# Optimization experiments

Measured on AMD Instinct MI355X. Metric: run time of the kernel, lower is better.

Reference implementation:

```python
import jax, jax.numpy as jnp
import numpy as np

B = 4096        # batch_size
D = 256         # feature_dim
N = 9000000     # dataset size (state buffer length)
G = 100         # num_groups
ALPHA = 0.5     # alpha_weight
GAMMA = 0.8
RHO = 8.0
LAM = 1.0       # lambada
ETA_P = 0.01
EPS = 1e-14
CLIP = 5.0


def setup_inputs() -> dict:
    key = jax.random.key(0)
    k = jax.random.split(key, 6)
    zis = jax.random.normal(k[0], (B, D), jnp.float32)
    zjs = jax.random.normal(k[1], (B, D), jnp.float32)
    # per-sample learned temperatures, small positive values
    taus_I = 0.01 + 0.2 * jax.random.uniform(k[2], (N,), jnp.float32)
    taus_T = 0.01 + 0.2 * jax.random.uniform(k[3], (N,), jnp.float32)
    group_info_I = jax.random.randint(k[4], (N,), 0, G, dtype=jnp.int32)
    group_info_T = jax.random.randint(k[5], (N,), 0, G, dtype=jnp.int32)
    ids = jnp.arange(B, dtype=jnp.int32)  # unique sample indices
    zeros_N = jnp.zeros((N,), jnp.float32)
    return {
        "zis": zis, "zjs": zjs,
        "s_I": zeros_N, "s_T": zeros_N, "b_I": zeros_N, "b_T": zeros_N,
        "z_I": jnp.zeros((G,), jnp.float32), "z_T": jnp.zeros((G,), jnp.float32),
        "p_I": jnp.ones((G,), jnp.float32) / G, "p_T": jnp.ones((G,), jnp.float32) / G,
        "taus_I": taus_I, "taus_T": taus_T,
        "ids": ids, "group_info_I": group_info_I, "group_info_T": group_info_T,
    }


def _l2norm(x):
    return x / jnp.maximum(jnp.linalg.norm(x, axis=1, keepdims=True), 1e-12)


def reference(zis, zjs, s_I, s_T, b_I, b_T, z_I, z_T, p_I, p_T,
              taus_I, taus_T, ids, group_info_I, group_info_T):
    zis = _l2norm(zis)
    zjs = _l2norm(zjs)
    sim = zis @ zjs.T                                   # [B, B]
    diag = jnp.diagonal(sim)                            # [B]
    mask_neg = 1.0 - jnp.eye(B, dtype=sim.dtype)
    image_diffs = sim - diag[:, None]
    text_diffs = sim - diag[None, :]

    tau_I = taus_I[ids]                                 # [B]
    tau_T = taus_T[ids]
    idt = jax.lax.stop_gradient(image_diffs / tau_I[:, None])
    tdt = jax.lax.stop_gradient(text_diffs / tau_T[None, :])

    # running max state (numerically-stable exp)
    old_b_I = b_I[ids]
    b_I_new = jnp.maximum(jnp.max(idt, axis=1), old_b_I)    # [B]
    old_b_T = b_T[ids]
    b_T_new = jnp.maximum(jnp.max(tdt, axis=0), old_b_T)    # [B]
    b_I = b_I.at[ids].set(b_I_new)
    b_T = b_T.at[ids].set(b_T_new)

    exp_I = jnp.exp(idt - b_I_new[:, None]) * mask_neg
    exp_T = jnp.exp(tdt - b_T_new[None, :]) * mask_neg
    g_I = jnp.sum(exp_I, axis=1)                         # [B]
    g_T = jnp.sum(exp_T, axis=0)                         # [B]

    # EMA of softmax denominators with max-rescaling
    s_I_new = (1.0 - GAMMA) * s_I[ids] * jnp.exp(old_b_I - b_I_new) + GAMMA * g_I
    s_T_new = (1.0 - GAMMA) * s_T[ids] * jnp.exp(old_b_T - b_T_new) + GAMMA * g_T
    s_I = s_I.at[ids].set(s_I_new)
    s_T = s_T.at[ids].set(s_T_new)
    s_I_c = jnp.maximum(s_I_new, EPS)
    s_T_c = jnp.maximum(s_T_new, EPS)

    w_I = exp_I / s_I_c[:, None]
    w_T = exp_T / s_T_c[None, :]

    gid_I = group_info_I[ids]                            # [B]
    gid_T = group_info_T[ids]
    gw_I = G * p_I[gid_I]                                # [B]
    gw_T = G * p_T[gid_T]

    image_loss = jnp.sum(w_I * gw_I[:, None] * image_diffs, axis=1)   # [B]
    text_loss = jnp.sum(w_T * gw_T[None, :] * text_diffs, axis=0)     # [B]
    total_loss = ALPHA * image_loss.mean() + (1.0 - ALPHA) * text_loss.mean()

    # per-group adversarial weight update
    F_I = tau_I * (jnp.log(s_I_c) + b_I_new + RHO)       # [B]
    F_T = tau_T * (jnp.log(s_T_c) + b_T_new + RHO)
    ones_b = jnp.ones((B,), sim.dtype)
    cnt_I = jnp.maximum(jax.ops.segment_sum(ones_b, gid_I, num_segments=G), 1.0)
    cnt_T = jnp.maximum(jax.ops.segment_sum(ones_b, gid_T, num_segments=G), 1.0)
    grad_p_I = jax.ops.segment_sum(F_I, gid_I, num_segments=G) / cnt_I
    grad_p_T = jax.ops.segment_sum(F_T, gid_T, num_segments=G) / cnt_T

    z_I = (1.0 - GAMMA) * z_I + GAMMA * grad_p_I
    z_T = (1.0 - GAMMA) * z_T + GAMMA * grad_p_T
    grad_hp_I = -LAM * jnp.log(p_I + EPS) - LAM
    grad_hp_T = -LAM * jnp.log(p_T + EPS) - LAM
    new_p_I = p_I * jnp.exp(2.0 * ETA_P * jnp.clip(z_I + grad_hp_I, -CLIP, CLIP))
    new_p_T = p_T * jnp.exp(2.0 * ETA_P * jnp.clip(z_T + grad_hp_T, -CLIP, CLIP))
    p_I = new_p_I / new_p_I.sum()
    p_T = new_p_T / new_p_T.sum()

    return total_loss, p_I, p_T
```

## Files before the change

kernel.cpp:

```cpp
#include <hip/hip_runtime.h>
#include <hip/hip_bf16.h>
#include <math.h>

#define BB 4096
#define DD 256
#define GG 100
#define GAMMA_C 0.8f
#define RHO_C 8.0f
#define ALPHA_C 0.5f
#define EPS_C 1e-14f
#define NS2 64

typedef __bf16 bf16x8 __attribute__((ext_vector_type(8)));
typedef float f32x4 __attribute__((ext_vector_type(4)));

__device__ inline void gl2lds16(const void* g, void* l) {
    __builtin_amdgcn_global_load_lds((__attribute__((address_space(1))) void*)(void*)g,
                                     (__attribute__((address_space(3))) void*)l, 16, 0, 0);
}

__device__ inline float blockReduceSum(float v, float* lds) {
    for (int o = 32; o > 0; o >>= 1) v += __shfl_down(v, o);
    int lane = threadIdx.x & 63, wid = threadIdx.x >> 6;
    if (lane == 0) lds[wid] = v;
    __syncthreads();
    if (threadIdx.x == 0) {
        float r = lds[0];
        int nw = blockDim.x >> 6;
        for (int w = 1; w < nw; w++) r += lds[w];
        lds[0] = r;
    }
    __syncthreads();
    float r = lds[0];
    __syncthreads();
    return r;
}

__global__ void norm_kernel(const float* __restrict__ zis,
                            const float* __restrict__ zjs,
                            ushort* __restrict__ zhi, ushort* __restrict__ zlo,
                            ushort* __restrict__ whi, ushort* __restrict__ wlo,
                            float* __restrict__ diag, float* __restrict__ acc) {
    __shared__ float lds[8];
    int r = blockIdx.x;
    if (r == 0) { acc[threadIdx.x] = 0.f; acc[threadIdx.x + 256] = 0.f; }
    float zv = zis[r * DD + threadIdx.x];
    float wv = zjs[r * DD + threadIdx.x];
    float sz = blockReduceSum(zv * zv, lds);
    float sw = blockReduceSum(wv * wv, lds);
    float nz = zv * (1.0f / fmaxf(sqrtf(sz), 1e-12f));
    float nw = wv * (1.0f / fmaxf(sqrtf(sw), 1e-12f));
    float dt = blockReduceSum(nz * nw, lds);
    if (threadIdx.x == 0) diag[r] = dt;
    __hip_bfloat16 hz = __float2bfloat16(nz);
    __hip_bfloat16 lz = __float2bfloat16(nz - __bfloat162float(hz));
    __hip_bfloat16 hw = __float2bfloat16(nw);
    __hip_bfloat16 lw = __float2bfloat16(nw - __bfloat162float(hw));
    zhi[r * DD + threadIdx.x] = *(ushort*)&hz;
    zlo[r * DD + threadIdx.x] = *(ushort*)&lz;
    whi[r * DD + threadIdx.x] = *(ushort*)&hw;
    wlo[r * DD + threadIdx.x] = *(ushort*)&lw;
}

__global__ void __launch_bounds__(256) fused_tile(const ushort* __restrict__ Ahi,
        const ushort* __restrict__ Alo, const ushort* __restrict__ Bhi,
        const ushort* __restrict__ Blo, const float* __restrict__ diag,
        const float* __restrict__ tausI, const float* __restrict__ tausT,
        const int* __restrict__ ids,
        float* __restrict__ pmR, float* __restrict__ pgR, float* __restrict__ pwR,
        float* __restrict__ pmC, float* __restrict__ pgC, float* __restrict__ pwC) {
    __shared__ ushort sAhi[128 * 32];
    __shared__ ushort sAlo[128 * 32];
    __shared__ ushort sBhi[128 * 32];
    __shared__ ushort sBlo[128 * 32];
    __shared__ float rDiag[128], rITau[128];
    __shared__ float cDiag[128], cITau[128];

    int lane = threadIdx.x & 63;
    int wv = threadIdx.x >> 6;
    int wm = wv >> 1, wn = wv & 1;
    int bm = blockIdx.y * 128, bn = blockIdx.x * 128;
    int ml = lane & 15, kq = lane >> 4;
    int koff = kq * 8;

    if (threadIdx.x < 128) {
        int r = bm + threadIdx.x;
        rDiag[threadIdx.x] = diag[r];
        rITau[threadIdx.x] = 1.0f / tausI[ids[r]];
    } else {
        int c = bn + threadIdx.x - 128;
        cDiag[threadIdx.x - 128] = diag[c];
        cITau[threadIdx.x - 128] = 1.0f / tausT[ids[c]];
    }

    f32x4 acc[4][4] = {};
    for (int k0 = 0; k0 < DD; k0 += 32) {
        for (int i = 0; i < 2; i++) {
            int cbase = i * 256 + wv * 64;
            int c = cbase + lane;
            int row = c >> 2;
            int col = (c & 3) * 8;
            size_t ga = (size_t)(bm + row) * DD + k0 + col;
            size_t gb = (size_t)(bn + row) * DD + k0 + col;
            int lofs = cbase * 8;
            gl2lds16(&Ahi[ga], &sAhi[lofs]);
            gl2lds16(&Alo[ga], &sAlo[lofs]);
            gl2lds16(&Bhi[gb], &sBhi[lofs]);
            gl2lds16(&Blo[gb], &sBlo[lofs]);
        }
        __syncthreads();
        bf16x8 ah[4], al[4], bh[4], bl[4];
        for (int t = 0; t < 4; t++) {
            int ar = wm * 64 + t * 16 + ml;
            ah[t] = *(const bf16x8*)&sAhi[ar * 32 + koff];
            al[t] = *(const bf16x8*)&sAlo[ar * 32 + koff];
            int br = wn * 64 + t * 16 + ml;
            bh[t] = *(const bf16x8*)&sBhi[br * 32 + koff];
            bl[t] = *(const bf16x8*)&sBlo[br * 32 + koff];
        }
        for (int t = 0; t < 4; t++)
            for (int u = 0; u < 4; u++) {
                acc[t][u] = __builtin_amdgcn_mfma_f32_16x16x32_bf16(ah[t], bh[u], acc[t][u], 0, 0, 0);
                acc[t][u] = __builtin_amdgcn_mfma_f32_16x16x32_bf16(ah[t], bl[u], acc[t][u], 0, 0, 0);
                acc[t][u] = __builtin_amdgcn_mfma_f32_16x16x32_bf16(al[t], bh[u], acc[t][u], 0, 0, 0);
            }
        __syncthreads();
    }

    float rd[4][4], rit[4][4];
    for (int t = 0; t < 4; t++)
        for (int reg = 0; reg < 4; reg++) {
            int rl = wm * 64 + t * 16 + kq * 4 + reg;
            rd[t][reg] = rDiag[rl];
            rit[t][reg] = rITau[rl];
        }
    float blocR[4][4];
    for (int t = 0; t < 4; t++)
        for (int reg = 0; reg < 4; reg++) {
            float m = fmaxf(fmaxf(acc[t][0][reg], acc[t][1][reg]),
                            fmaxf(acc[t][2][reg], acc[t][3][reg]));
            for (int mask = 1; mask <= 8; mask <<= 1)
                m = fmaxf(m, __shfl_xor(m, mask));
            blocR[t][reg] = (m - rd[t][reg]) * rit[t][reg];
        }
    float cd[4], cit[4], cbloc[4];
    for (int u = 0; u < 4; u++) {
        int cl = wn * 64 + u * 16 + ml;
        cd[u] = cDiag[cl];
        cit[u] = cITau[cl];
        float m = -INFINITY;
        for (int t = 0; t < 4; t++)
            for (int reg = 0; reg < 4; reg++)
                m = fmaxf(m, acc[t][u][reg]);
        for (int mask = 16; mask <= 32; mask <<= 1)
            m = fmaxf(m, __shfl_xor(m, mask));
        cbloc[u] = (m - cd[u]) * cit[u];
    }
    float rg[4][4] = {}, rw[4][4] = {}, cg[4] = {}, cw[4] = {};
    for (int t = 0; t < 4; t++) {
        int gr0 = bm + wm * 64 + t * 16 + kq * 4;
        for (int u = 0; u < 4; u++) {
            int gc = bn + wn * 64 + u * 16 + ml;
            for (int reg = 0; reg < 4; reg++) {
                float v = acc[t][u][reg];
                bool off = (gr0 + reg) != gc;
                float dvI = v - rd[t][reg];
                float eI = off ? __expf(dvI * rit[t][reg] - blocR[t][reg]) : 0.f;
                rg[t][reg] += eI;
                rw[t][reg] += eI * dvI;
                float dvT = v - cd[u];
                float eT = off ? __expf(dvT * cit[u] - cbloc[u]) : 0.f;
                cg[u] += eT;
                cw[u] += eT * dvT;
            }
        }
    }
    int stripeR = blockIdx.x * 2 + wn;
    for (int t = 0; t < 4; t++) {
        for (int reg = 0; reg < 4; reg++)
            for (int mask = 1; mask <= 8; mask <<= 1) {
                rg[t][reg] += __shfl_xor(rg[t][reg], mask);
                rw[t][reg] += __shfl_xor(rw[t][reg], mask);
            }
        if (ml == 0) {
            size_t o = (size_t)stripeR * BB + bm + wm * 64 + t * 16 + kq * 4;
            *(float4*)&pmR[o] = make_float4(blocR[t][0], blocR[t][1], blocR[t][2], blocR[t][3]);
            *(float4*)&pgR[o] = make_float4(rg[t][0], rg[t][1], rg[t][2], rg[t][3]);
            *(float4*)&pwR[o] = make_float4(rw[t][0], rw[t][1], rw[t][2], rw[t][3]);
        }
    }
    int stripeC = blockIdx.y * 2 + wm;
    for (int u = 0; u < 4; u++) {
        for (int mask = 16; mask <= 32; mask <<= 1) {
            cg[u] += __shfl_xor(cg[u], mask);
            cw[u] += __shfl_xor(cw[u], mask);
        }
        if (kq == 0) {
            size_t o = (size_t)stripeC * BB + bn + wn * 64 + u * 16 + ml;
            pmC[o] = cbloc[u];
            pgC[o] = cg[u];
            pwC[o] = cw[u];
        }
    }
}

__global__ void __launch_bounds__(256) fin_kernel(
        const float* __restrict__ pmR, const float* __restrict__ pgR,
        const float* __restrict__ pwR, const float* __restrict__ pmC,
        const float* __restrict__ pgC, const float* __restrict__ pwC,
        const float* __restrict__ sI, const float* __restrict__ bI,
        const float* __restrict__ tausI, const int* __restrict__ gInfI,
        const float* __restrict__ pI,
        const float* __restrict__ sT, const float* __restrict__ bT,
        const float* __restrict__ tausT, const int* __restrict__ gInfT,
        const float* __restrict__ pT,
        const int* __restrict__ ids, float* __restrict__ acc) {
    __shared__ float lds[8];
    __shared__ float binF[GG], binC[GG];
    if (threadIdx.x < GG) { binF[threadIdx.x] = 0.f; binC[threadIdx.x] = 0.f; }
    __syncthreads();
    int side = blockIdx.x >> 4;
    int i = (blockIdx.x & 15) * 256 + threadIdx.x;
    const float* pm = side ? pmC : pmR;
    const float* pg = side ? pgC : pgR;
    const float* pw = side ? pwC : pwR;
    const float* sS = side ? sT : sI;
    const float* bS = side ? bT : bI;
    const float* taus = side ? tausT : tausI;
    const int* ginfo = side ? gInfT : gInfI;
    const float* pP = side ? pT : pI;

    int id = ids[i];
    float oldb = bS[id];
    float m = -INFINITY;
    for (int s = 0; s < NS2; s++) m = fmaxf(m, pm[(size_t)s * BB + i]);
    float bfin = fmaxf(m, oldb);
    float g = 0.f, wsum = 0.f;
    for (int s = 0; s < NS2; s++) {
        float f = __expf(pm[(size_t)s * BB + i] - bfin);
        g += pg[(size_t)s * BB + i] * f;
        wsum += pw[(size_t)s * BB + i] * f;
    }
    float tau = taus[id];
    float snew = (1.f - GAMMA_C) * sS[id] * expf(oldb - bfin) + GAMMA_C * g;
    float sc = fmaxf(snew, EPS_C);
    int gid = ginfo[id];
    float gw = (float)GG * pP[gid];
    float loss = gw * wsum / sc;
    float F = tau * (logf(sc) + bfin + RHO_C);
    atomicAdd(&binF[gid], F);
    atomicAdd(&binC[gid], 1.0f);
    float lsum = blockReduceSum(loss, lds);
    if (threadIdx.x == 0) atomicAdd(&acc[side], lsum);
    __syncthreads();
    if (threadIdx.x < GG) {
        atomicAdd(&acc[2 + side * 200 + threadIdx.x], binF[threadIdx.x]);
        atomicAdd(&acc[102 + side * 200 + threadIdx.x], binC[threadIdx.x]);
    }
}

__global__ void final_kernel(const float* __restrict__ acc,
                             const float* __restrict__ zI, const float* __restrict__ zT,
                             const float* __restrict__ pI, const float* __restrict__ pT,
                             float* __restrict__ out) {
    __shared__ float sumsI[2], sumsT[2];
    int g = threadIdx.x;
    float npI = 0.f, npT = 0.f;
    if (g < GG) {
        float cntI = fmaxf(acc[102 + g], 1.f);
        float gpI = acc[2 + g] / cntI;
        float zi = (1.f - GAMMA_C) * zI[g] + GAMMA_C * gpI;
        float ghpI = -logf(pI[g] + EPS_C) - 1.f;
        float ti = fminf(fmaxf(zi + ghpI, -5.f), 5.f);
        npI = pI[g] * expf(0.02f * ti);

        float cntT = fmaxf(acc[302 + g], 1.f);
        float gpT = acc[202 + g] / cntT;
        float zt = (1.f - GAMMA_C) * zT[g] + GAMMA_C * gpT;
        float ghpT = -logf(pT[g] + EPS_C) - 1.f;
        float tt = fminf(fmaxf(zt + ghpT, -5.f), 5.f);
        npT = pT[g] * expf(0.02f * tt);
    }
    float vI = npI, vT = npT;
    for (int o = 32; o > 0; o >>= 1) {
        vI += __shfl_down(vI, o);
        vT += __shfl_down(vT, o);
    }
    int wid = threadIdx.x >> 6, lane = threadIdx.x & 63;
    if (lane == 0) { sumsI[wid] = vI; sumsT[wid] = vT; }
    __syncthreads();
    float sumI = sumsI[0] + sumsI[1];
    float sumT = sumsT[0] + sumsT[1];
    if (g < GG) {
        out[1 + g] = npI / sumI;
        out[101 + g] = npT / sumT;
    }
    if (threadIdx.x == 0) {
        out[0] = ALPHA_C * (acc[0] / (float)BB) + (1.f - ALPHA_C) * (acc[1] / (float)BB);
    }
}

extern "C" void kernel_launch(void* const* d_in, const int* in_sizes, int n_in,
                              void* d_out, int out_size, void* d_ws, size_t ws_size,
                              hipStream_t stream) {
    const float* zis   = (const float*)d_in[0];
    const float* zjs   = (const float*)d_in[1];
    const float* s_I   = (const float*)d_in[2];
    const float* s_T   = (const float*)d_in[3];
    const float* b_I   = (const float*)d_in[4];
    const float* b_T   = (const float*)d_in[5];
    const float* z_I   = (const float*)d_in[6];
    const float* z_T   = (const float*)d_in[7];
    const float* p_I   = (const float*)d_in[8];
    const float* p_T   = (const float*)d_in[9];
    const float* tausI = (const float*)d_in[10];
    const float* tausT = (const float*)d_in[11];
    const int*   ids   = (const int*)d_in[12];
    const int*   gInfI = (const int*)d_in[13];
    const int*   gInfT = (const int*)d_in[14];
    float* out = (float*)d_out;

    char* ws = (char*)d_ws;
    ushort* zhi = (ushort*)ws;
    ushort* zlo = zhi + (size_t)BB * DD;
    ushort* whi = zlo + (size_t)BB * DD;
    ushort* wlo = whi + (size_t)BB * DD;
    float* acc  = (float*)(wlo + (size_t)BB * DD);
    float* diag = acc + 512;
    float* pmR  = diag + BB;
    float* pgR  = pmR + (size_t)NS2 * BB;
    float* pwR  = pgR + (size_t)NS2 * BB;
    float* pmC  = pwR + (size_t)NS2 * BB;
    float* pgC  = pmC + (size_t)NS2 * BB;
    float* pwC  = pgC + (size_t)NS2 * BB;

    norm_kernel<<<BB, 256, 0, stream>>>(zis, zjs, zhi, zlo, whi, wlo, diag, acc);
    fused_tile<<<dim3(32, 32), 256, 0, stream>>>(zhi, zlo, whi, wlo, diag,
            tausI, tausT, ids, pmR, pgR, pwR, pmC, pgC, pwC);
    fin_kernel<<<32, 256, 0, stream>>>(pmR, pgR, pwR, pmC, pgC, pwC,
            s_I, b_I, tausI, gInfI, p_I, s_T, b_T, tausT, gInfT, p_T, ids, acc);
    final_kernel<<<1, 128, 0, stream>>>(acc, z_I, z_T, p_I, p_T, out);
}
```

Baseline: 321.4 us.

## Pre-swizzle bf16 operands into MFMA fragment order and load directly from global

```diff
diff --git a/kernel.cpp b/kernel.cpp
--- a/kernel.cpp
+++ b/kernel.cpp
@@ -14,9 +14,9 @@
 typedef __bf16 bf16x8 __attribute__((ext_vector_type(8)));
 typedef float f32x4 __attribute__((ext_vector_type(4)));
 
-__device__ inline void gl2lds16(const void* g, void* l) {
-    __builtin_amdgcn_global_load_lds((__attribute__((address_space(1))) void*)(void*)g,
-                                     (__attribute__((address_space(3))) void*)l, 16, 0, 0);
+__device__ inline int swz(int r, int k) {
+    return ((r >> 4) << 12) | ((k >> 5) << 9) | (((k >> 3) & 3) << 7) |
+           ((r & 15) << 3) | (k & 7);
 }
 
 __device__ inline float blockReduceSum(float v, float* lds) {
@@ -56,10 +56,11 @@
     __hip_bfloat16 lz = __float2bfloat16(nz - __bfloat162float(hz));
     __hip_bfloat16 hw = __float2bfloat16(nw);
     __hip_bfloat16 lw = __float2bfloat16(nw - __bfloat162float(hw));
-    zhi[r * DD + threadIdx.x] = *(ushort*)&hz;
-    zlo[r * DD + threadIdx.x] = *(ushort*)&lz;
-    whi[r * DD + threadIdx.x] = *(ushort*)&hw;
-    wlo[r * DD + threadIdx.x] = *(ushort*)&lw;
+    int si = swz(r, threadIdx.x);
+    zhi[si] = *(ushort*)&hz;
+    zlo[si] = *(ushort*)&lz;
+    whi[si] = *(ushort*)&hw;
+    wlo[si] = *(ushort*)&lw;
 }
 
 __global__ void __launch_bounds__(256) fused_tile(const ushort* __restrict__ Ahi,
@@ -69,10 +70,6 @@
         const int* __restrict__ ids,
         float* __restrict__ pmR, float* __restrict__ pgR, float* __restrict__ pwR,
         float* __restrict__ pmC, float* __restrict__ pgC, float* __restrict__ pwC) {
-    __shared__ ushort sAhi[128 * 32];
-    __shared__ ushort sAlo[128 * 32];
-    __shared__ ushort sBhi[128 * 32];
-    __shared__ ushort sBlo[128 * 32];
     __shared__ float rDiag[128], rITau[128];
     __shared__ float cDiag[128], cITau[128];
 
@@ -81,7 +78,6 @@
     int wm = wv >> 1, wn = wv & 1;
     int bm = blockIdx.y * 128, bn = blockIdx.x * 128;
     int ml = lane & 15, kq = lane >> 4;
-    int koff = kq * 8;
 
     if (threadIdx.x < 128) {
         int r = bm + threadIdx.x;
@@ -93,39 +89,32 @@
         cITau[threadIdx.x - 128] = 1.0f / tausT[ids[c]];
     }
 
+    int aBlk = (bm >> 4) + wm * 4;
+    int bBlk = (bn >> 4) + wn * 4;
+    int lofs = lane * 8;
+
     f32x4 acc[4][4] = {};
-    for (int k0 = 0; k0 < DD; k0 += 32) {
-        for (int i = 0; i < 2; i++) {
-            int cbase = i * 256 + wv * 64;
-            int c = cbase + lane;
-            int row = c >> 2;
-            int col = (c & 3) * 8;
-            size_t ga = (size_t)(bm + row) * DD + k0 + col;
-            size_t gb = (size_t)(bn + row) * DD + k0 + col;
-            int lofs = cbase * 8;
-            gl2lds16(&Ahi[ga], &sAhi[lofs]);
-            gl2lds16(&Alo[ga], &sAlo[lofs]);
-            gl2lds16(&Bhi[gb], &sBhi[lofs]);
-            gl2lds16(&Blo[gb], &sBlo[lofs]);
-        }
-        __syncthreads();
+#pragma unroll
+    for (int s = 0; s < 8; s++) {
+        int so = s * 512 + lofs;
         bf16x8 ah[4], al[4], bh[4], bl[4];
+#pragma unroll
         for (int t = 0; t < 4; t++) {
-            int ar = wm * 64 + t * 16 + ml;
-            ah[t] = *(const bf16x8*)&sAhi[ar * 32 + koff];
-            al[t] = *(const bf16x8*)&sAlo[ar * 32 + koff];
-            int br = wn * 64 + t * 16 + ml;
-            bh[t] = *(const bf16x8*)&sBhi[br * 32 + koff];
-            bl[t] = *(const bf16x8*)&sBlo[br * 32 + koff];
-        }
+            ah[t] = *(const bf16x8*)&Ahi[(aBlk + t) * 4096 + so];
+            al[t] = *(const bf16x8*)&Alo[(aBlk + t) * 4096 + so];
+            bh[t] = *(const bf16x8*)&Bhi[(bBlk + t) * 4096 + so];
+            bl[t] = *(const bf16x8*)&Blo[(bBlk + t) * 4096 + so];
+        }
+#pragma unroll
         for (int t = 0; t < 4; t++)
+#pragma unroll
             for (int u = 0; u < 4; u++) {
                 acc[t][u] = __builtin_amdgcn_mfma_f32_16x16x32_bf16(ah[t], bh[u], acc[t][u], 0, 0, 0);
                 acc[t][u] = __builtin_amdgcn_mfma_f32_16x16x32_bf16(ah[t], bl[u], acc[t][u], 0, 0, 0);
                 acc[t][u] = __builtin_amdgcn_mfma_f32_16x16x32_bf16(al[t], bh[u], acc[t][u], 0, 0, 0);
             }
-        __syncthreads();
-    }
+    }
+    __syncthreads();
 
     float rd[4][4], rit[4][4];
     for (int t = 0; t < 4; t++)
```

Result: no change. 327.1 us (+1.8%).
